# Kernel optimization log

Hardware: AMD Instinct MI355X
Metric: run time of the kernel (lower is better)

Reference implementation:

```python
import jax, jax.numpy as jnp
import numpy as np

N_NODES = 50000
HEADS = 3
C = 64  # node_channels
NEG_SLOPE = 0.2


def setup_inputs() -> dict:
    key = jax.random.key(0)
    ks = jax.random.split(key, 8)
    E = 800000
    x = jax.random.normal(ks[0], (N_NODES, C), dtype=jnp.float32)
    edge_index = jax.random.randint(ks[1], (2, E), 0, N_NODES, dtype=jnp.int64)
    edge_attr = jax.random.normal(ks[2], (E, 16), dtype=jnp.float32)
    weight_node = jax.random.normal(ks[3], (C, HEADS * C), dtype=jnp.float32) * 0.1
    weight_edge = jax.random.normal(ks[4], (16, HEADS * C), dtype=jnp.float32) * 0.1
    weight_triplet_att = jax.random.normal(ks[5], (1, HEADS, 3 * C), dtype=jnp.float32) * 0.1
    weight_scale = jax.random.normal(ks[6], (HEADS * C, C), dtype=jnp.float32) * 0.1
    bias = jnp.zeros((C,), dtype=jnp.float32)
    return {"x": x, "edge_index": edge_index, "edge_attr": edge_attr,
            "weight_node": weight_node, "weight_edge": weight_edge,
            "weight_triplet_att": weight_triplet_att,
            "weight_scale": weight_scale, "bias": bias}


def reference(x, edge_index, edge_attr, weight_node, weight_edge,
              weight_triplet_att, weight_scale, bias):
    E = edge_index.shape[1]
    src = edge_index[0]  # j (source)
    dst = edge_index[1]  # i (target, softmax/aggregation index)

    x_proj = x @ weight_node              # [N, H*C]
    e = edge_attr @ weight_edge           # [E, H*C]

    x_j = x_proj[src].reshape(E, HEADS, C)
    x_i = x_proj[dst].reshape(E, HEADS, C)
    e_ij = e.reshape(E, HEADS, C)

    # attention weights split over the triplet concat [x_i | e_ij | x_j]
    w = weight_triplet_att.reshape(HEADS, 3, C)  # [H,3,C]
    alpha = (jnp.einsum('ehc,hc->eh', x_i, w[:, 0])
             + jnp.einsum('ehc,hc->eh', e_ij, w[:, 1])
             + jnp.einsum('ehc,hc->eh', x_j, w[:, 2]))  # [E,H]
    alpha = jnp.where(alpha >= 0, alpha, NEG_SLOPE * alpha)  # leaky_relu

    # scatter-softmax over incoming edges of each target node
    m = jax.ops.segment_max(alpha, dst, num_segments=N_NODES)  # [N,H]
    m = jnp.where(jnp.isfinite(m), m, 0.0)
    exp_a = jnp.exp(alpha - m[dst])
    denom = jax.ops.segment_sum(exp_a, dst, num_segments=N_NODES)  # [N,H]
    alpha = exp_a / (denom[dst] + 1e-16)

    msg = alpha[:, :, None] * e_ij * x_j  # [E,H,C]
    aggr = jax.ops.segment_sum(msg.reshape(E, HEADS * C), dst,
                               num_segments=N_NODES)  # [N,H*C]
    return aggr @ weight_scale + bias
```

## Files before the change

kernel.cpp:

```cpp
#include <hip/hip_runtime.h>
#include <hip/hip_bf16.h>


#define N_NODES 50000
#define CCH 64
#define HEADS 3
#define HC 192
#define NEG_SLOPE 0.2f
#define NWAVES 12288

typedef _Float16 h2 __attribute__((ext_vector_type(2)));
__device__ __forceinline__ h2 uh(unsigned u) {
    union { unsigned u; h2 h; } x; x.u = u; return x.h;
}
__device__ __forceinline__ unsigned hu(float a, float b) {
    union { unsigned u; _Float16 h[2]; } x;
    x.h[0] = (_Float16)a; x.h[1] = (_Float16)b; return x.u;
}

__global__ void k_prep(const float* __restrict__ We, const float* __restrict__ Watt,
                       float* __restrict__ v1) {
    int t = threadIdx.x;
    if (t >= HEADS * 16) return;
    int h = t / 16, k = t % 16;
    float s = 0.f;
    #pragma unroll
    for (int c = 0; c < CCH; ++c)
        s = fmaf(We[k * HC + h * CCH + c], Watt[h * HC + CCH + c], s);
    v1[t] = s;
}

__global__ __launch_bounds__(192) void k_xproj(
    const float* __restrict__ x, const float* __restrict__ Wn,
    const float* __restrict__ Watt, uint2* __restrict__ xph2,
    float* __restrict__ a0, float* __restrict__ a2) {
    __shared__ float xs[16 * CCH];
    __shared__ _Float16 pack[16 * CCH * 4];
    int t = threadIdx.x;
    float wreg[CCH];
    #pragma unroll
    for (int k = 0; k < CCH; ++k) wreg[k] = Wn[k * HC + t];
    int base = blockIdx.x * 16;
    for (int i = t; i < 16 * CCH; i += 192) {
        int idx = base * CCH + i;
        xs[i] = (idx < N_NODES * CCH) ? x[idx] : 0.f;
    }
    __syncthreads();
    int h = t >> 6, c = t & 63;
    float w0 = Watt[h * HC + c];
    float w2 = Watt[h * HC + 2 * CCH + c];
    #pragma unroll 1
    for (int j = 0; j < 16; ++j) {
        int n = base + j;
        if (n >= N_NODES) break;
        float val = 0.f;
        #pragma unroll
        for (int k = 0; k < CCH; k += 4) {
            float4 xv = *(const float4*)&xs[j * CCH + k];
            val = fmaf(xv.x, wreg[k], val);
            val = fmaf(xv.y, wreg[k + 1], val);
            val = fmaf(xv.z, wreg[k + 2], val);
            val = fmaf(xv.w, wreg[k + 3], val);
        }
        pack[(j * CCH + c) * 4 + h] = (_Float16)val;
        if (h == 0) pack[(j * CCH + c) * 4 + 3] = (_Float16)0.f;
        float p0 = val * w0, p2 = val * w2;
        #pragma unroll
        for (int off = 32; off; off >>= 1) {
            p0 += __shfl_down(p0, off);
            p2 += __shfl_down(p2, off);
        }
        if (c == 0) { a0[n * HEADS + h] = p0; a2[n * HEADS + h] = p2; }
    }
    __syncthreads();
    const uint2* p2v = (const uint2*)pack;
    for (int i = t; i < 16 * CCH; i += 192) {
        int n = base + (i >> 6);
        if (n < N_NODES) xph2[(size_t)base * CCH + i] = p2v[i];
    }
}

__global__ __launch_bounds__(256) void k_hist(const int* __restrict__ ei,
                                              int* __restrict__ cnt, int E) {
    int e = blockIdx.x * 256 + threadIdx.x;
    if (e < E) atomicAdd(&cnt[ei[E + e]], 1);
}

__global__ __launch_bounds__(1024) void k_bsum(const int* __restrict__ cnt,
                                               int* __restrict__ bsum) {
    __shared__ int ws[16];
    int t = threadIdx.x, lane = t & 63, wid = t >> 6;
    int i = blockIdx.x * 1024 + t;
    int v = (i < N_NODES) ? cnt[i] : 0;
    #pragma unroll
    for (int o = 32; o; o >>= 1) v += __shfl_down(v, o);
    if (lane == 0) ws[wid] = v;
    __syncthreads();
    if (wid == 0) {
        int s = (lane < 16) ? ws[lane] : 0;
        #pragma unroll
        for (int o = 8; o; o >>= 1) s += __shfl_down(s, o);
        if (lane == 0) bsum[blockIdx.x] = s;
    }
}

__global__ __launch_bounds__(64) void k_bscan(const int* __restrict__ bsum,
                                              int* __restrict__ boff,
                                              int* __restrict__ off) {
    int t = threadIdx.x;
    int v = (t < 49) ? bsum[t] : 0;
    int x = v;
    #pragma unroll
    for (int o = 1; o < 64; o <<= 1) {
        int y = __shfl_up(x, o);
        if (t >= o) x += y;
    }
    if (t < 49) boff[t] = x - v;
    if (t == 48) off[N_NODES] = x;
}

__global__ __launch_bounds__(1024) void k_fin(const int* __restrict__ cnt,
                                              const int* __restrict__ boff,
                                              int* __restrict__ off,
                                              int* __restrict__ cursor) {
    __shared__ int ws[16];
    int t = threadIdx.x, lane = t & 63, wid = t >> 6;
    int i = blockIdx.x * 1024 + t;
    int v = (i < N_NODES) ? cnt[i] : 0;
    int x = v;
    #pragma unroll
    for (int o = 1; o < 64; o <<= 1) {
        int y = __shfl_up(x, o);
        if (lane >= o) x += y;
    }
    if (lane == 63) ws[wid] = x;
    __syncthreads();
    if (wid == 0) {
        int s = (lane < 16) ? ws[lane] : 0;
        #pragma unroll
        for (int o = 1; o < 16; o <<= 1) {
            int y = __shfl_up(s, o);
            if (lane >= o) s += y;
        }
        if (lane < 16) ws[lane] = s;
    }
    __syncthreads();
    int excl = boff[blockIdx.x] + (wid ? ws[wid - 1] : 0) + x - v;
    if (i < N_NODES) { off[i] = excl; cursor[i] = excl; }
}

__global__ __launch_bounds__(256) void k_part(const int* __restrict__ off,
                                              int* __restrict__ wstart, int E) {
    int w = blockIdx.x * 256 + threadIdx.x;
    if (w > NWAVES) return;
    if (w == NWAVES) { wstart[NWAVES] = N_NODES; return; }
    long tgt = (long)E * w / NWAVES;
    int lo = 0, hi = N_NODES;
    while (lo < hi) {
        int mid = (lo + hi) >> 1;
        if (off[mid] < (int)tgt) lo = mid + 1; else hi = mid;
    }
    wstart[w] = lo;
}

__global__ __launch_bounds__(256) void k_place(
    const int* __restrict__ ei, const float* __restrict__ ea,
    const float* __restrict__ a0, const float* __restrict__ a2,
    const float* __restrict__ v1, int* __restrict__ cursor,
    float* __restrict__ recs, int E) {
    __shared__ float v1s[48];
    if (threadIdx.x < 48) v1s[threadIdx.x] = v1[threadIdx.x];
    __syncthreads();
    int e = blockIdx.x * 256 + threadIdx.x;
    if (e >= E) return;
    int src = ei[e], dst = ei[E + e];
    const float4* q = (const float4*)(ea + (size_t)e * 16);
    float4 q0 = q[0], q1 = q[1], q2 = q[2], q3 = q[3];
    float at[16] = {q0.x, q0.y, q0.z, q0.w, q1.x, q1.y, q1.z, q1.w,
                    q2.x, q2.y, q2.z, q2.w, q3.x, q3.y, q3.z, q3.w};
    float ex[HEADS];
    #pragma unroll
    for (int h = 0; h < HEADS; ++h) {
        float s = a0[dst * HEADS + h] + a2[src * HEADS + h];
        #pragma unroll
        for (int j = 0; j < 16; ++j) s = fmaf(at[j], v1s[h * 16 + j], s);
        s = (s >= 0.f) ? s : NEG_SLOPE * s;
        ex[h] = __expf(s);
    }
    int pos = atomicAdd(&cursor[dst], 1);
    float* rp = recs + (size_t)pos * 12;
    uint4 r0 = {hu(at[0], at[1]), hu(at[2], at[3]), hu(at[4], at[5]), hu(at[6], at[7])};
    uint4 r1 = {hu(at[8], at[9]), hu(at[10], at[11]), hu(at[12], at[13]), hu(at[14], at[15])};
    float4 r2 = {ex[0], ex[1], ex[2], __int_as_float(src)};
    *(uint4*)rp = r0;
    *(uint4*)(rp + 4) = r1;
    *(float4*)(rp + 8) = r2;
}

__global__ __launch_bounds__(256, 6) void k_msg(
    const int* __restrict__ off, const int* __restrict__ wstart,
    const float* __restrict__ recs, const uint2* __restrict__ xph2,
    const float* __restrict__ We, _Float16* __restrict__ rowsH) {
    int lane = threadIdx.x & 63;
    int w = blockIdx.x * 4 + (threadIdx.x >> 6);
    #define WP(h, q) hu(We[(2*(q)) * HC + (h) * CCH + lane], \
                        We[(2*(q)+1) * HC + (h) * CCH + lane])
    unsigned w00 = WP(0,0), w01 = WP(0,1), w02 = WP(0,2), w03 = WP(0,3),
             w04 = WP(0,4), w05 = WP(0,5), w06 = WP(0,6), w07 = WP(0,7);
    unsigned w10 = WP(1,0), w11 = WP(1,1), w12 = WP(1,2), w13 = WP(1,3),
             w14 = WP(1,4), w15 = WP(1,5), w16 = WP(1,6), w17 = WP(1,7);
    unsigned w20 = WP(2,0), w21 = WP(2,1), w22 = WP(2,2), w23 = WP(2,3),
             w24 = WP(2,4), w25 = WP(2,5), w26 = WP(2,6), w27 = WP(2,7);
    #undef WP

    int n0 = wstart[w], n1 = wstart[w + 1];
    n0 = __builtin_amdgcn_readfirstlane(n0);
    n1 = __builtin_amdgcn_readfirstlane(n1);
    if (n0 >= n1) return;

    int n = n0;
    int k    = __builtin_amdgcn_readfirstlane(off[n0]);
    int kend = __builtin_amdgcn_readfirstlane(off[n1]);
    int re   = __builtin_amdgcn_readfirstlane(off[n0 + 1]);

    float acc0 = 0.f, acc1 = 0.f, acc2 = 0.f;
    float den0 = 0.f, den1 = 0.f, den2 = 0.f;

    uint4 U0, U1; float4 RX; uint2 xv;
    if (k < kend) {
        const float* rp = recs + (size_t)k * 12;
        U0 = *(const uint4*)rp;
        U1 = *(const uint4*)(rp + 4);
        RX = *(const float4*)(rp + 8);
        int src = __builtin_amdgcn_readfirstlane(__float_as_int(RX.w));
        xv = xph2[(size_t)src * CCH + lane];
    }

    #define FLUSH(nn)                                                      \
        {                                                                  \
            size_t ro = (size_t)(nn) * HC + lane;                          \
            rowsH[ro]           = (_Float16)(acc0 / (den0 + 1e-16f));      \
            rowsH[ro + CCH]     = (_Float16)(acc1 / (den1 + 1e-16f));      \
            rowsH[ro + 2 * CCH] = (_Float16)(acc2 / (den2 + 1e-16f));      \
            acc0 = acc1 = acc2 = den0 = den1 = den2 = 0.f;                 \
        }

    while (k < kend) {
        while (k == re) {
            FLUSH(n);
            ++n;
            re = __builtin_amdgcn_readfirstlane(off[n + 1]);
        }
        int kn = (k + 1 < kend) ? k + 1 : k;
        const float* rpn = recs + (size_t)kn * 12;
        uint4 U0n = *(const uint4*)rpn;
        uint4 U1n = *(const uint4*)(rpn + 4);
        float4 RXn = *(const float4*)(rpn + 8);
        float ev0 = 0.f, ev1 = 0.f, ev2 = 0.f;
        #define D(u, wv, acc) acc = __builtin_amdgcn_fdot2(uh(u), uh(wv), acc, false);
        D(U0.x, w00, ev0) D(U0.x, w10, ev1) D(U0.x, w20, ev2)
        D(U0.y, w01, ev0) D(U0.y, w11, ev1) D(U0.y, w21, ev2)
        D(U0.z, w02, ev0) D(U0.z, w12, ev1) D(U0.z, w22, ev2)
        D(U0.w, w03, ev0) D(U0.w, w13, ev1) D(U0.w, w23, ev2)
        D(U1.x, w04, ev0) D(U1.x, w14, ev1) D(U1.x, w24, ev2)
        D(U1.y, w05, ev0) D(U1.y, w15, ev1) D(U1.y, w25, ev2)
        D(U1.z, w06, ev0) D(U1.z, w16, ev1) D(U1.z, w26, ev2)
        D(U1.w, w07, ev0) D(U1.w, w17, ev1) D(U1.w, w27, ev2)
        #undef D
        h2 xa = uh(xv.x), xb = uh(xv.y);
        den0 += RX.x; den1 += RX.y; den2 += RX.z;
        acc0 = fmaf(RX.x * ev0, (float)xa.x, acc0);
        acc1 = fmaf(RX.y * ev1, (float)xa.y, acc1);
        acc2 = fmaf(RX.z * ev2, (float)xb.x, acc2);
        U0 = U0n; U1 = U1n; RX = RXn;
        int src_n = __builtin_amdgcn_readfirstlane(__float_as_int(RXn.w));
        xv = xph2[(size_t)src_n * CCH + lane];
        ++k;
    }
    FLUSH(n);
    while (++n < n1) FLUSH(n);
    #undef FLUSH
}

__global__ __launch_bounds__(512) void k_out(
    const _Float16* __restrict__ rowsH, const float* __restrict__ Ws,
    const float* __restrict__ bias, float* __restrict__ out) {
    __shared__ float wss[HC * CCH];
    __shared__ float rtile[8 * HC];
    int t = threadIdx.x, wid = t >> 6, c = t & 63;
    {
        float4* d4 = (float4*)wss;
        const float4* s4 = (const float4*)Ws;
        for (int i = t; i < HC * CCH / 4; i += 512) d4[i] = s4[i];
    }
    float b = bias[c];
    int base = blockIdx.x * 200;
    #pragma unroll 1
    for (int it = 0; it < 25; ++it) {
        int gbase = base + it * 8;
        int vn = N_NODES - gbase;
        vn = vn < 0 ? 0 : (vn > 8 ? 8 : vn);
        int vu = vn * (HC / 2);
        __syncthreads();
        const unsigned* rg = (const unsigned*)(rowsH + (size_t)gbase * HC);
        for (int i = t; i < 8 * HC / 2; i += 512) {
            h2 v = (i < vu) ? uh(rg[i]) : uh(0u);
            rtile[2 * i]     = (float)v.x;
            rtile[2 * i + 1] = (float)v.y;
        }
        __syncthreads();
        int n = gbase + wid;
        if (n < N_NODES) {
            float val = b;
            #pragma unroll
            for (int k = 0; k < HC; k += 4) {
                float4 r = *(const float4*)&rtile[wid * HC + k];
                val = fmaf(r.x, wss[k * CCH + c], val);
                val = fmaf(r.y, wss[(k + 1) * CCH + c], val);
                val = fmaf(r.z, wss[(k + 2) * CCH + c], val);
                val = fmaf(r.w, wss[(k + 3) * CCH + c], val);
            }
            out[(size_t)n * CCH + c] = val;
        }
    }
}

extern "C" void kernel_launch(void* const* d_in, const int* in_sizes, int n_in,
                              void* d_out, int out_size, void* d_ws, size_t ws_size,
                              hipStream_t stream) {
    const float* x    = (const float*)d_in[0];
    const int*   ei   = (const int*)d_in[1];
    const float* ea   = (const float*)d_in[2];
    const float* Wn   = (const float*)d_in[3];
    const float* We   = (const float*)d_in[4];
    const float* Watt = (const float*)d_in[5];
    const float* Ws   = (const float*)d_in[6];
    const float* bias = (const float*)d_in[7];
    float* out = (float*)d_out;

    const int E = in_sizes[1] / 2;

    char* w = (char*)d_ws;
    size_t o = 0;
    int*   cnt    = (int*)(w + o);    o += 50048 * 4;
    int*   off    = (int*)(w + o);    o += 50064 * 4;
    int*   cursor = (int*)(w + o);    o += 50048 * 4;
    int*   wst    = (int*)(w + o);    o += (NWAVES + 16) * 4;
    int*   bsum   = (int*)(w + o);    o += 64 * 4;
    int*   boff   = (int*)(w + o);    o += 64 * 4;
    float* v1     = (float*)(w + o);  o += 64 * 4;
    float* a0     = (float*)(w + o);  o += 150016 * 4;
    float* a2     = (float*)(w + o);  o += 150016 * 4;
    uint2* xph2   = (uint2*)(w + o);  o += (size_t)N_NODES * CCH * 8;
    _Float16* rowsH = (_Float16*)(w + o); o += (size_t)N_NODES * HC * 2;
    float* recs   = (float*)(w + o);  o += (size_t)E * 48;

    hipMemsetAsync(cnt, 0, 50048 * 4, stream);

    k_prep<<<1, 64, 0, stream>>>(We, Watt, v1);
    k_xproj<<<(N_NODES + 15) / 16, 192, 0, stream>>>(x, Wn, Watt, xph2, a0, a2);
    k_hist<<<(E + 255) / 256, 256, 0, stream>>>(ei, cnt, E);
    k_bsum<<<49, 1024, 0, stream>>>(cnt, bsum);
    k_bscan<<<1, 64, 0, stream>>>(bsum, boff, off);
    k_fin<<<49, 1024, 0, stream>>>(cnt, boff, off, cursor);
    k_part<<<(NWAVES + 256) / 256, 256, 0, stream>>>(off, wst, E);
    k_place<<<(E + 255) / 256, 256, 0, stream>>>(ei, ea, a0, a2, v1, cursor, recs, E);
    k_msg<<<NWAVES / 4, 256, 0, stream>>>(off, wst, recs, xph2, We, rowsH);
    k_out<<<250, 512, 0, stream>>>(rowsH, Ws, bias, out);
}
```

Baseline: 411.4 us.

## Fuse small prep kernels, rewrite output projection with fp16 dot2 registers

```diff
diff --git a/kernel.cpp b/kernel.cpp
--- a/kernel.cpp
+++ b/kernel.cpp
@@ -18,50 +18,43 @@
     x.h[0] = (_Float16)a; x.h[1] = (_Float16)b; return x.u;
 }
 
-__global__ void k_prep(const float* __restrict__ We, const float* __restrict__ Watt,
-                       float* __restrict__ v1) {
-    int t = threadIdx.x;
-    if (t >= HEADS * 16) return;
-    int h = t / 16, k = t % 16;
-    float s = 0.f;
-    #pragma unroll
-    for (int c = 0; c < CCH; ++c)
-        s = fmaf(We[k * HC + h * CCH + c], Watt[h * HC + CCH + c], s);
-    v1[t] = s;
+__global__ __launch_bounds__(256) void k_hist(const int* __restrict__ ei,
+                                              int* __restrict__ cnt,
+                                              const float* __restrict__ We,
+                                              const float* __restrict__ Watt,
+                                              float* __restrict__ v1, int E) {
+    int e = blockIdx.x * 256 + threadIdx.x;
+    if (e < E) atomicAdd(&cnt[ei[E + e]], 1);
+    if (blockIdx.x == 0 && threadIdx.x < HEADS * 16) {
+        int h = threadIdx.x / 16, k = threadIdx.x % 16;
+        float s = 0.f;
+        #pragma unroll
+        for (int c = 0; c < CCH; ++c)
+            s = fmaf(We[k * HC + h * CCH + c], Watt[h * HC + CCH + c], s);
+        v1[threadIdx.x] = s;
+    }
 }
 
 __global__ __launch_bounds__(192) void k_xproj(
     const float* __restrict__ x, const float* __restrict__ Wn,
     const float* __restrict__ Watt, uint2* __restrict__ xph2,
     float* __restrict__ a0, float* __restrict__ a2) {
-    __shared__ float xs[16 * CCH];
     __shared__ _Float16 pack[16 * CCH * 4];
     int t = threadIdx.x;
     float wreg[CCH];
     #pragma unroll
     for (int k = 0; k < CCH; ++k) wreg[k] = Wn[k * HC + t];
     int base = blockIdx.x * 16;
-    for (int i = t; i < 16 * CCH; i += 192) {
-        int idx = base * CCH + i;
-        xs[i] = (idx < N_NODES * CCH) ? x[idx] : 0.f;
-    }
-    __syncthreads();
     int h = t >> 6, c = t & 63;
     float w0 = Watt[h * HC + c];
     float w2 = Watt[h * HC + 2 * CCH + c];
+    int jmax = N_NODES - base; jmax = jmax > 16 ? 16 : jmax;
     #pragma unroll 1
-    for (int j = 0; j < 16; ++j) {
-        int n = base + j;
-        if (n >= N_NODES) break;
+    for (int j = 0; j < jmax; ++j) {
+        const float* xr = x + (size_t)(base + j) * CCH;
         float val = 0.f;
         #pragma unroll
-        for (int k = 0; k < CCH; k += 4) {
-            float4 xv = *(const float4*)&xs[j * CCH + k];
-            val = fmaf(xv.x, wreg[k], val);
-            val = fmaf(xv.y, wreg[k + 1], val);
-            val = fmaf(xv.z, wreg[k + 2], val);
-            val = fmaf(xv.w, wreg[k + 3], val);
-        }
+        for (int k = 0; k < CCH; ++k) val = fmaf(xr[k], wreg[k], val);
         pack[(j * CCH + c) * 4 + h] = (_Float16)val;
         if (h == 0) pack[(j * CCH + c) * 4 + 3] = (_Float16)0.f;
         float p0 = val * w0, p2 = val * w2;
@@ -70,7 +63,10 @@
             p0 += __shfl_down(p0, off);
             p2 += __shfl_down(p2, off);
         }
-        if (c == 0) { a0[n * HEADS + h] = p0; a2[n * HEADS + h] = p2; }
+        if (c == 0) {
+            a0[(base + j) * HEADS + h] = p0;
+            a2[(base + j) * HEADS + h] = p2;
+        }
     }
     __syncthreads();
     const uint2* p2v = (const uint2*)pack;
@@ -78,12 +74,6 @@
         int n = base + (i >> 6);
         if (n < N_NODES) xph2[(size_t)base * CCH + i] = p2v[i];
     }
-}
-
-__global__ __launch_bounds__(256) void k_hist(const int* __restrict__ ei,
-                                              int* __restrict__ cnt, int E) {
-    int e = blockIdx.x * 256 + threadIdx.x;
-    if (e < E) atomicAdd(&cnt[ei[E + e]], 1);
 }
 
 __global__ __launch_bounds__(1024) void k_bsum(const int* __restrict__ cnt,
@@ -104,26 +94,12 @@
     }
 }
 
-__global__ __launch_bounds__(64) void k_bscan(const int* __restrict__ bsum,
-                                              int* __restrict__ boff,
-                                              int* __restrict__ off) {
-    int t = threadIdx.x;
-    int v = (t < 49) ? bsum[t] : 0;
-    int x = v;
-    #pragma unroll
-    for (int o = 1; o < 64; o <<= 1) {
-        int y = __shfl_up(x, o);
-        if (t >= o) x += y;
-    }
-    if (t < 49) boff[t] = x - v;
-    if (t == 48) off[N_NODES] = x;
-}
-
 __global__ __launch_bounds__(1024) void k_fin(const int* __restrict__ cnt,
-                                              const int* __restrict__ boff,
+                                              const int* __restrict__ bsum,
                                               int* __restrict__ off,
                                               int* __restrict__ cursor) {
     __shared__ int ws[16];
+    __shared__ int bof_s;
     int t = threadIdx.x, lane = t & 63, wid = t >> 6;
     int i = blockIdx.x * 1024 + t;
     int v = (i < N_NODES) ? cnt[i] : 0;
@@ -143,9 +119,19 @@
             if (lane >= o) s += y;
         }
         if (lane < 16) ws[lane] = s;
+    } else if (wid == 1) {
+        int bv = (lane < 49) ? bsum[lane] : 0;
+        int bx = bv;
+        #pragma unroll
+        for (int o = 1; o < 64; o <<= 1) {
+            int y = __shfl_up(bx, o);
+            if (lane >= o) bx += y;
+        }
+        if (lane == (int)blockIdx.x) bof_s = bx - bv;
+        if (blockIdx.x == 48 && lane == 48) off[N_NODES] = bx;
     }
     __syncthreads();
-    int excl = boff[blockIdx.x] + (wid ? ws[wid - 1] : 0) + x - v;
+    int excl = bof_s + (wid ? ws[wid - 1] : 0) + x - v;
     if (i < N_NODES) { off[i] = excl; cursor[i] = excl; }
 }
 
@@ -168,9 +154,6 @@
     const float* __restrict__ a0, const float* __restrict__ a2,
     const float* __restrict__ v1, int* __restrict__ cursor,
     float* __restrict__ recs, int E) {
-    __shared__ float v1s[48];
-    if (threadIdx.x < 48) v1s[threadIdx.x] = v1[threadIdx.x];
-    __syncthreads();
     int e = blockIdx.x * 256 + threadIdx.x;
     if (e >= E) return;
     int src = ei[e], dst = ei[E + e];
@@ -183,7 +166,7 @@
     for (int h = 0; h < HEADS; ++h) {
         float s = a0[dst * HEADS + h] + a2[src * HEADS + h];
         #pragma unroll
-        for (int j = 0; j < 16; ++j) s = fmaf(at[j], v1s[h * 16 + j], s);
+        for (int j = 0; j < 16; ++j) s = fmaf(at[j], v1[h * 16 + j], s);
         s = (s >= 0.f) ? s : NEG_SLOPE * s;
         ex[h] = __expf(s);
     }
@@ -282,46 +265,57 @@
     #undef FLUSH
 }
 
-__global__ __launch_bounds__(512) void k_out(
+__global__ __launch_bounds__(256) void k_out(
     const _Float16* __restrict__ rowsH, const float* __restrict__ Ws,
     const float* __restrict__ bias, float* __restrict__ out) {
-    __shared__ float wss[HC * CCH];
-    __shared__ float rtile[8 * HC];
-    int t = threadIdx.x, wid = t >> 6, c = t & 63;
-    {
-        float4* d4 = (float4*)wss;
-        const float4* s4 = (const float4*)Ws;
-        for (int i = t; i < HC * CCH / 4; i += 512) d4[i] = s4[i];
-    }
-    float b = bias[c];
-    int base = blockIdx.x * 200;
+    int lane = threadIdx.x & 63;
+    int wgid = __builtin_amdgcn_readfirstlane(blockIdx.x * 4 + (threadIdx.x >> 6));
+    float b = bias[lane];
+    #define WQ(q) hu(Ws[(2*(q)) * CCH + lane], Ws[(2*(q)+1) * CCH + lane])
+    unsigned s00=WQ(0),  s01=WQ(1),  s02=WQ(2),  s03=WQ(3),  s04=WQ(4),  s05=WQ(5),  s06=WQ(6),  s07=WQ(7);
+    unsigned s08=WQ(8),  s09=WQ(9),  s10=WQ(10), s11=WQ(11), s12=WQ(12), s13=WQ(13), s14=WQ(14), s15=WQ(15);
+    unsigned s16=WQ(16), s17=WQ(17), s18=WQ(18), s19=WQ(19), s20=WQ(20), s21=WQ(21), s22=WQ(22), s23=WQ(23);
+    unsigned s24=WQ(24), s25=WQ(25), s26=WQ(26), s27=WQ(27), s28=WQ(28), s29=WQ(29), s30=WQ(30), s31=WQ(31);
+    unsigned s32=WQ(32), s33=WQ(33), s34=WQ(34), s35=WQ(35), s36=WQ(36), s37=WQ(37), s38=WQ(38), s39=WQ(39);
+    unsigned s40=WQ(40), s41=WQ(41), s42=WQ(42), s43=WQ(43), s44=WQ(44), s45=WQ(45), s46=WQ(46), s47=WQ(47);
+    unsigned s48=WQ(48), s49=WQ(49), s50=WQ(50), s51=WQ(51), s52=WQ(52), s53=WQ(53), s54=WQ(54), s55=WQ(55);
+    unsigned s56=WQ(56), s57=WQ(57), s58=WQ(58), s59=WQ(59), s60=WQ(60), s61=WQ(61), s62=WQ(62), s63=WQ(63);
+    unsigned s64=WQ(64), s65=WQ(65), s66=WQ(66), s67=WQ(67), s68=WQ(68), s69=WQ(69), s70=WQ(70), s71=WQ(71);
+    unsigned s72=WQ(72), s73=WQ(73), s74=WQ(74), s75=WQ(75), s76=WQ(76), s77=WQ(77), s78=WQ(78), s79=WQ(79);
+    unsigned s80=WQ(80), s81=WQ(81), s82=WQ(82), s83=WQ(83), s84=WQ(84), s85=WQ(85), s86=WQ(86), s87=WQ(87);
+    unsigned s88=WQ(88), s89=WQ(89), s90=WQ(90), s91=WQ(91), s92=WQ(92), s93=WQ(93), s94=WQ(94), s95=WQ(95);
+    #undef WQ
     #pragma unroll 1
-    for (int it = 0; it < 25; ++it) {
-        int gbase = base + it * 8;
-        int vn = N_NODES - gbase;
-        vn = vn < 0 ? 0 : (vn > 8 ? 8 : vn);
-        int vu = vn * (HC / 2);
-        __syncthreads();
-        const unsigned* rg = (const unsigned*)(rowsH + (size_t)gbase * HC);
-        for (int i = t; i < 8 * HC / 2; i += 512) {
-            h2 v = (i < vu) ? uh(rg[i]) : uh(0u);
-            rtile[2 * i]     = (float)v.x;
-            rtile[2 * i + 1] = (float)v.y;
-        }
-        __syncthreads();
-        int n = gbase + wid;
-        if (n < N_NODES) {
-            float val = b;
-            #pragma unroll
-            for (int k = 0; k < HC; k += 4) {
-                float4 r = *(const float4*)&rtile[wid * HC + k];
-                val = fmaf(r.x, wss[k * CCH + c], val);
-                val = fmaf(r.y, wss[(k + 1) * CCH + c], val);
-                val = fmaf(r.z, wss[(k + 2) * CCH + c], val);
-                val = fmaf(r.w, wss[(k + 3) * CCH + c], val);
-            }
-            out[(size_t)n * CCH + c] = val;
-        }
+    for (int n = wgid; n < N_NODES; n += 1024) {
+        const unsigned* rp = (const unsigned*)(rowsH + (size_t)n * HC);
+        float a0_ = b, a1_ = 0.f, a2_ = 0.f, a3_ = 0.f;
+        #define DQ(q, sreg, acc) acc = __builtin_amdgcn_fdot2(uh(rp[q]), uh(sreg), acc, false);
+        DQ(0,s00,a0_)  DQ(1,s01,a1_)  DQ(2,s02,a2_)  DQ(3,s03,a3_)
+        DQ(4,s04,a0_)  DQ(5,s05,a1_)  DQ(6,s06,a2_)  DQ(7,s07,a3_)
+        DQ(8,s08,a0_)  DQ(9,s09,a1_)  DQ(10,s10,a2_) DQ(11,s11,a3_)
+        DQ(12,s12,a0_) DQ(13,s13,a1_) DQ(14,s14,a2_) DQ(15,s15,a3_)
+        DQ(16,s16,a0_) DQ(17,s17,a1_) DQ(18,s18,a2_) DQ(19,s19,a3_)
+        DQ(20,s20,a0_) DQ(21,s21,a1_) DQ(22,s22,a2_) DQ(23,s23,a3_)
+        DQ(24,s24,a0_) DQ(25,s25,a1_) DQ(26,s26,a2_) DQ(27,s27,a3_)
+        DQ(28,s28,a0_) DQ(29,s29,a1_) DQ(30,s30,a2_) DQ(31,s31,a3_)
+        DQ(32,s32,a0_) DQ(33,s33,a1_) DQ(34,s34,a2_) DQ(35,s35,a3_)
+        DQ(36,s36,a0_) DQ(37,s37,a1_) DQ(38,s38,a2_) DQ(39,s39,a3_)
+        DQ(40,s40,a0_) DQ(41,s41,a1_) DQ(42,s42,a2_) DQ(43,s43,a3_)
+        DQ(44,s44,a0_) DQ(45,s45,a1_) DQ(46,s46,a2_) DQ(47,s47,a3_)
+        DQ(48,s48,a0_) DQ(49,s49,a1_) DQ(50,s50,a2_) DQ(51,s51,a3_)
+        DQ(52,s52,a0_) DQ(53,s53,a1_) DQ(54,s54,a2_) DQ(55,s55,a3_)
+        DQ(56,s56,a0_) DQ(57,s57,a1_) DQ(58,s58,a2_) DQ(59,s59,a3_)
+        DQ(60,s60,a0_) DQ(61,s61,a1_) DQ(62,s62,a2_) DQ(63,s63,a3_)
+        DQ(64,s64,a0_) DQ(65,s65,a1_) DQ(66,s66,a2_) DQ(67,s67,a3_)
+        DQ(68,s68,a0_) DQ(69,s69,a1_) DQ(70,s70,a2_) DQ(71,s71,a3_)
+        DQ(72,s72,a0_) DQ(73,s73,a1_) DQ(74,s74,a2_) DQ(75,s75,a3_)
+        DQ(76,s76,a0_) DQ(77,s77,a1_) DQ(78,s78,a2_) DQ(79,s79,a3_)
+        DQ(80,s80,a0_) DQ(81,s81,a1_) DQ(82,s82,a2_) DQ(83,s83,a3_)
+        DQ(84,s84,a0_) DQ(85,s85,a1_) DQ(86,s86,a2_) DQ(87,s87,a3_)
+        DQ(88,s88,a0_) DQ(89,s89,a1_) DQ(90,s90,a2_) DQ(91,s91,a3_)
+        DQ(92,s92,a0_) DQ(93,s93,a1_) DQ(94,s94,a2_) DQ(95,s95,a3_)
+        #undef DQ
+        out[(size_t)n * CCH + lane] = (a0_ + a1_) + (a2_ + a3_);
     }
 }
 
@@ -347,7 +341,6 @@
     int*   cursor = (int*)(w + o);    o += 50048 * 4;
     int*   wst    = (int*)(w + o);    o += (NWAVES + 16) * 4;
     int*   bsum   = (int*)(w + o);    o += 64 * 4;
-    int*   boff   = (int*)(w + o);    o += 64 * 4;
     float* v1     = (float*)(w + o);  o += 64 * 4;
     float* a0     = (float*)(w + o);  o += 150016 * 4;
     float* a2     = (float*)(w + o);  o += 150016 * 4;
@@ -357,14 +350,12 @@
 
     hipMemsetAsync(cnt, 0, 50048 * 4, stream);
 
-    k_prep<<<1, 64, 0, stream>>>(We, Watt, v1);
+    k_hist<<<(E + 255) / 256, 256, 0, stream>>>(ei, cnt, We, Watt, v1, E);
     k_xproj<<<(N_NODES + 15) / 16, 192, 0, stream>>>(x, Wn, Watt, xph2, a0, a2);
-    k_hist<<<(E + 255) / 256, 256, 0, stream>>>(ei, cnt, E);
     k_bsum<<<49, 1024, 0, stream>>>(cnt, bsum);
-    k_bscan<<<1, 64, 0, stream>>>(bsum, boff, off);
-    k_fin<<<49, 1024, 0, stream>>>(cnt, boff, off, cursor);
+    k_fin<<<49, 1024, 0, stream>>>(cnt, bsum, off, cursor);
     k_part<<<(NWAVES + 256) / 256, 256, 0, stream>>>(off, wst, E);
     k_place<<<(E + 255) / 256, 256, 0, stream>>>(ei, ea, a0, a2, v1, cursor, recs, E);
     k_msg<<<NWAVES / 4, 256, 0, stream>>>(off, wst, recs, xph2, We, rowsH);
-    k_out<<<250, 512, 0, stream>>>(rowsH, Ws, bias, out);
-}
+    k_out<<<256, 256, 0, stream>>>(rowsH, Ws, bias, out);
+}
```

Result: faster. 377.2 us (-8.3%).
